# Performance work log

Measured on AMD Instinct MI355X. Metric: run time of the kernel, lower is better.

Reference implementation:

```python
import jax, jax.numpy as jnp
import numpy as np

EPS = 1e-5

def layernorm(x, g, b):
    mu = jnp.mean(x, axis=-1, keepdims=True)
    var = jnp.mean(jnp.square(x - mu), axis=-1, keepdims=True)
    return (x - mu) * jax.lax.rsqrt(var + EPS) * g + b

def setup_inputs() -> dict:
    key = jax.random.key(0)
    ks = jax.random.split(key, 12)
    B, V, P, C = 2, 8192, 16, 256
    FFN_IN, FFN_HID = 2 * C, 2 * C * 4
    s = 0.02
    return {
        "source": jax.random.normal(ks[0], (B, V, C), jnp.float32),
        "target": jax.random.normal(ks[1], (B, V, P, C), jnp.float32),
        "weights": jax.random.uniform(ks[2], (B, V, P), jnp.float32),
        "confidences": jax.random.uniform(ks[3], (B, V, P), jnp.float32),
        "Wq": jax.random.normal(ks[4], (C, C), jnp.float32) * s,
        "Wk": jax.random.normal(ks[5], (C, C), jnp.float32) * s,
        "Wv": jax.random.normal(ks[6], (C, C), jnp.float32) * s,
        "Wm": jax.random.normal(ks[7], (C, C), jnp.float32) * s,
        "g1": jnp.ones((C,), jnp.float32),
        "b1": jnp.zeros((C,), jnp.float32),
        "Wf1": jax.random.normal(ks[8], (FFN_IN, FFN_HID), jnp.float32) * s,
        "Wf2": jax.random.normal(ks[9], (FFN_HID, C), jnp.float32) * s,
        "g2": jnp.ones((C,), jnp.float32),
        "b2": jnp.zeros((C,), jnp.float32),
    }

NUM_HEAD = 8

def reference(source, target, weights, confidences, Wq, Wk, Wv, Wm, g1, b1, Wf1, Wf2, g2, b2):
    B, V, P, C = target.shape
    H = NUM_HEAD
    D = C // H
    # projections (bias-free linears)
    q = (source @ Wq).reshape(B, V, H, D)          # [B,V,H,D]
    k = (target @ Wk).reshape(B, V, P, H, D)       # [B,V,P,H,D]
    v = (target @ Wv).reshape(B, V, P, H, D)
    # scores scaled by per-neighbor weights then softmax over P
    scores = jnp.einsum("bvhd,bvphd->bvhp", q, k) * weights[:, :, None, :] / jnp.sqrt(jnp.float32(D))
    attn = jax.nn.softmax(scores, axis=-1)          # [B,V,H,P]
    # confidence-scaled weighted sum over neighbors
    out = jnp.einsum("bvhp,bvp,bvphd->bvhd", attn, confidences, v).reshape(B, V, C)
    message = layernorm(out @ Wm, g1, b1)
    h = jnp.concatenate([source, message], axis=-1) @ Wf1
    message = layernorm(jax.nn.gelu(h, approximate=False) @ Wf2, g2, b2)
    return source + message
```

## Files before the change

### kernel.cpp

```cpp
#include <hip/hip_runtime.h>
#include <hip/hip_bf16.h>
#include <math.h>

#define T_TOK 16384
#define CC 256
#define PP 16
#define HH 8
#define DD 32
#define LN_EPS 1e-5f

typedef __attribute__((ext_vector_type(8))) short bf16x8_t;
typedef __attribute__((ext_vector_type(4))) float f32x4_t;

__device__ __forceinline__ unsigned short f2bf(float x) {
  __hip_bfloat16 h = __float2bfloat16(x);
  return *reinterpret_cast<unsigned short*>(&h);
}
__device__ __forceinline__ float bf2f(unsigned short u) {
  union { unsigned int i; float f; } v; v.i = ((unsigned int)u) << 16; return v.f;
}
__device__ __forceinline__ void gl_lds16(const unsigned short* g, unsigned short* l) {
  __builtin_amdgcn_global_load_lds(
      (const __attribute__((address_space(1))) unsigned int*)g,
      (__attribute__((address_space(3))) unsigned int*)l, 16, 0, 0);
}

__global__ __launch_bounds__(256) void cvt_bf16_kernel(const float* __restrict__ src,
                                                       unsigned short* __restrict__ dst) {
  int i = (blockIdx.x * 256 + threadIdx.x) * 4;
  float4 v = *(const float4*)&src[i];
  ushort4 o = make_ushort4(f2bf(v.x), f2bf(v.y), f2bf(v.z), f2bf(v.w));
  *(ushort4*)&dst[i] = o;
}

__global__ __launch_bounds__(256) void transpose_cvt_kernel(const float* __restrict__ src,
                                                            unsigned short* __restrict__ dst,
                                                            int K, int N) {
  __shared__ float tile[64][65];
  int k0 = blockIdx.x * 64, n0 = blockIdx.y * 64;
  int tid = threadIdx.x;
#pragma unroll
  for (int i = 0; i < 16; i++) {
    int lin = i * 256 + tid, r = lin >> 6, c = lin & 63;
    tile[r][c] = src[(size_t)(k0 + r) * N + n0 + c];
  }
  __syncthreads();
#pragma unroll
  for (int i = 0; i < 16; i++) {
    int lin = i * 256 + tid, n = lin >> 6, k = lin & 63;
    dst[(size_t)(n0 + n) * K + k0 + k] = f2bf(tile[k][n]);
  }
}

__global__ __launch_bounds__(256) void precM_kernel(const float* __restrict__ Wq,
                                                    const float* __restrict__ Wk,
                                                    unsigned short* __restrict__ Mt) {
  __shared__ float wqS[256][33];
  __shared__ float wkS[128][33];
  const int tid = threadIdx.x;
  const int h = blockIdx.x >> 1, eh = blockIdx.x & 1;
#pragma unroll
  for (int it = 0; it < 32; it++) {
    int lin = it * 256 + tid, r = lin >> 5, d = lin & 31;
    wqS[r][d] = Wq[(size_t)r * CC + h * DD + d];
  }
#pragma unroll
  for (int it = 0; it < 16; it++) {
    int lin = it * 256 + tid, r = lin >> 5, d = lin & 31;
    wkS[r][d] = Wk[(size_t)(eh * 128 + r) * CC + h * DD + d];
  }
  __syncthreads();
  const int w = tid >> 6, l = tid & 63;
  for (int ei = 0; ei < 32; ei++) {
    int e = w * 32 + ei;
    float o[4] = {0.f, 0.f, 0.f, 0.f};
#pragma unroll
    for (int d = 0; d < 32; d++) {
      float kv = wkS[e][d];
      o[0] += kv * wqS[l][d];
      o[1] += kv * wqS[l + 64][d];
      o[2] += kv * wqS[l + 128][d];
      o[3] += kv * wqS[l + 192][d];
    }
    size_t rowb = (size_t)(h * 256 + eh * 128 + e) * CC;
    Mt[rowb + l] = f2bf(o[0]);
    Mt[rowb + l + 64] = f2bf(o[1]);
    Mt[rowb + l + 128] = f2bf(o[2]);
    Mt[rowb + l + 192] = f2bf(o[3]);
  }
}

__global__ __launch_bounds__(256) void precWVM_kernel(const float* __restrict__ Wv,
                                                      const float* __restrict__ Wm,
                                                      unsigned short* __restrict__ WVMt) {
  __shared__ float WvS[256][33];
  __shared__ float WmS[32][257];
  const int h = blockIdx.x;
  const int tid = threadIdx.x;
#pragma unroll
  for (int it = 0; it < 32; it++) {
    int lin = it * 256 + tid, e = lin >> 5, d = lin & 31;
    WvS[e][d] = Wv[(size_t)e * CC + h * DD + d];
  }
#pragma unroll
  for (int it = 0; it < 32; it++) {
    int lin = it * 256 + tid, d = lin >> 8, c = lin & 255;
    WmS[d][c] = Wm[(size_t)(h * DD + d) * CC + c];
  }
  __syncthreads();
  float wm[32];
#pragma unroll
  for (int d = 0; d < 32; d++) wm[d] = WmS[d][tid];
  for (int e = 0; e < 256; e++) {
    float acc = 0.f;
#pragma unroll
    for (int d = 0; d < 32; d++) acc += WvS[e][d] * wm[d];
    WVMt[(size_t)tid * 2048 + h * 256 + e] = f2bf(acc);
  }
}

__global__ __launch_bounds__(512) void qk_gemm_kernel(
    const unsigned short* __restrict__ A, const unsigned short* __restrict__ Bt,
    unsigned short* __restrict__ Out, int K, int strideO) {
  __shared__ __align__(16) unsigned short As[64 * 64];
  __shared__ __align__(16) unsigned short Bs[256 * 64];
  const int tid = threadIdx.x;
  const int wv = tid >> 6, l = tid & 63;
  const int wr = wv >> 2, wc = wv & 3;
  const int lr = l & 15, lq = l >> 4;
  const int m0 = blockIdx.x * 64;
  const int n0 = blockIdx.y * 256;
  const int nsteps = K >> 6;

  f32x4_t acc[2][4];
#pragma unroll
  for (int m = 0; m < 2; m++)
#pragma unroll
    for (int n = 0; n < 4; n++) acc[m][n] = (f32x4_t){0.f, 0.f, 0.f, 0.f};

  const int rS = tid >> 3, sS = tid & 7, qS = sS ^ (rS & 7);

  for (int st = 0; st < nsteps; st++) {
    int kn = st * 64;
    gl_lds16(&A[(size_t)(m0 + rS) * K + kn + qS * 8], &As[tid * 8]);
#pragma unroll
    for (int it = 0; it < 4; it++) {
      int lin = it * 512 + tid, r = lin >> 3, s = lin & 7, q = s ^ (r & 7);
      gl_lds16(&Bt[(size_t)(n0 + r) * K + kn + q * 8], &Bs[lin * 8]);
    }
    __syncthreads();
#pragma unroll
    for (int kk = 0; kk < 2; kk++) {
      bf16x8_t af[2], bfr[4];
#pragma unroll
      for (int m = 0; m < 2; m++) {
        int r = wr * 32 + m * 16 + lr;
        int slot = (kk * 4 + lq) ^ (r & 7);
        af[m] = *(const bf16x8_t*)&As[r * 64 + slot * 8];
      }
#pragma unroll
      for (int n = 0; n < 4; n++) {
        int r = wc * 64 + n * 16 + lr;
        int slot = (kk * 4 + lq) ^ (r & 7);
        bfr[n] = *(const bf16x8_t*)&Bs[r * 64 + slot * 8];
      }
#pragma unroll
      for (int m = 0; m < 2; m++)
#pragma unroll
        for (int n = 0; n < 4; n++)
          acc[m][n] = __builtin_amdgcn_mfma_f32_16x16x32_bf16(af[m], bfr[n], acc[m][n], 0, 0, 0);
    }
    __syncthreads();
  }

#pragma unroll
  for (int m = 0; m < 2; m++)
#pragma unroll
    for (int n = 0; n < 4; n++)
#pragma unroll
      for (int j = 0; j < 4; j++) {
        int rl = wr * 32 + m * 16 + lq * 4 + j;
        int col = n0 + wc * 64 + n * 16 + lr;
        Out[(size_t)(m0 + rl) * strideO + col] = f2bf(acc[m][n][j]);
      }
}

__global__ __launch_bounds__(256) void gemm128_kernel(
    const unsigned short* __restrict__ A, const unsigned short* __restrict__ A2,
    const unsigned short* __restrict__ Bt, unsigned short* __restrict__ Out,
    int K, int strideO) {
  __shared__ __align__(16) unsigned short As[128 * 64];
  __shared__ __align__(16) unsigned short Bs[128 * 64];
  const int tid = threadIdx.x;
  const int wv = tid >> 6, l = tid & 63;
  const int wr = wv >> 1, wc = wv & 1;
  const int lr = l & 15, lq = l >> 4;
  const int m0 = blockIdx.x * 128;
  const int n0 = blockIdx.y * 128;
  const int nsteps = K >> 6;

  f32x4_t acc[4][4];
#pragma unroll
  for (int m = 0; m < 4; m++)
#pragma unroll
    for (int n = 0; n < 4; n++) acc[m][n] = (f32x4_t){0.f, 0.f, 0.f, 0.f};

  for (int st = 0; st < nsteps; st++) {
    int kn = st * 64;
#pragma unroll
    for (int it = 0; it < 4; it++) {
      int lin = it * 256 + tid, r = lin >> 3, s = lin & 7, q = s ^ (r & 7);
      int ka = kn + q * 8;
      const unsigned short* ap = (ka < 256) ? &A[(size_t)(m0 + r) * CC + ka]
                                            : &A2[(size_t)(m0 + r) * CC + ka - 256];
      gl_lds16(ap, &As[lin * 8]);
      gl_lds16(&Bt[(size_t)(n0 + r) * K + kn + q * 8], &Bs[lin * 8]);
    }
    __syncthreads();
#pragma unroll
    for (int kk = 0; kk < 2; kk++) {
      bf16x8_t af[4], bf[4];
#pragma unroll
      for (int m = 0; m < 4; m++) {
        int r = wr * 64 + m * 16 + lr;
        int slot = (kk * 4 + lq) ^ (r & 7);
        af[m] = *(const bf16x8_t*)&As[r * 64 + slot * 8];
      }
#pragma unroll
      for (int n = 0; n < 4; n++) {
        int r = wc * 64 + n * 16 + lr;
        int slot = (kk * 4 + lq) ^ (r & 7);
        bf[n] = *(const bf16x8_t*)&Bs[r * 64 + slot * 8];
      }
#pragma unroll
      for (int m = 0; m < 4; m++)
#pragma unroll
        for (int n = 0; n < 4; n++)
          acc[m][n] = __builtin_amdgcn_mfma_f32_16x16x32_bf16(af[m], bf[n], acc[m][n], 0, 0, 0);
    }
    __syncthreads();
  }

#pragma unroll
  for (int m = 0; m < 4; m++)
#pragma unroll
    for (int n = 0; n < 4; n++)
#pragma unroll
      for (int j = 0; j < 4; j++) {
        int row = m0 + wr * 64 + m * 16 + lq * 4 + j;
        int col = n0 + wc * 64 + n * 16 + lr;
        float x = acc[m][n][j];
        x = 0.5f * x * (1.0f + erff(x * 0.70710678118654752f));
        Out[(size_t)row * strideO + col] = f2bf(x);
      }
}

__global__ __launch_bounds__(256) void attn2_kernel(const unsigned short* __restrict__ QKc,
                                                    const float* __restrict__ target,
                                                    const float* __restrict__ wts,
                                                    const float* __restrict__ conf,
                                                    unsigned short* __restrict__ TC) {
  __shared__ __align__(16) unsigned short Ts[4][16 * 256];
  __shared__ float awL[4][PP][HH];
  const int tid = threadIdx.x;
  const int w = tid >> 6, l = tid & 63;
  const int t = blockIdx.x * 4 + w;
  const float* trow = target + (size_t)t * PP * CC;
  char* tsb = (char*)&Ts[w][0];

  {
    const int p = l >> 2;
#pragma unroll
    for (int i = 0; i < 8; i++) {
      int s = (l & 3) + i * 4;
      const float* gp = &trow[p * CC + s * 8];
      float4 v0 = *(const float4*)gp;
      float4 v1 = *(const float4*)(gp + 4);
      ushort4 u0 = make_ushort4(f2bf(v0.x), f2bf(v0.y), f2bf(v0.z), f2bf(v0.w));
      ushort4 u1 = make_ushort4(f2bf(v1.x), f2bf(v1.y), f2bf(v1.z), f2bf(v1.w));
      uint4 pk;
      pk.x = (unsigned)u0.x | ((unsigned)u0.y << 16);
      pk.y = (unsigned)u0.z | ((unsigned)u0.w << 16);
      pk.z = (unsigned)u1.x | ((unsigned)u1.y << 16);
      pk.w = (unsigned)u1.z | ((unsigned)u1.w << 16);
      *(uint4*)(tsb + p * 512 + ((s ^ (p & 7)) << 4)) = pk;
    }
  }

  f32x4_t sc4 = (f32x4_t){0.f, 0.f, 0.f, 0.f};
  {
    const int lr = l & 15, lq = l >> 4;
    const unsigned short* qkrow = QKc + (size_t)t * 2048 + (size_t)(lr & 7) * 256;
#pragma unroll
    for (int es = 0; es < 8; es++) {
      int slot = es * 4 + lq;
      bf16x8_t aF = *(const bf16x8_t*)(tsb + lr * 512 + ((slot ^ (lr & 7)) << 4));
      bf16x8_t bF = *(const bf16x8_t*)&qkrow[es * 32 + lq * 8];
      sc4 = __builtin_amdgcn_mfma_f32_16x16x32_bf16(aF, bF, sc4, 0, 0, 0);
    }
  }

  {
    const int g = l >> 4;
    const float rsD = 0.17677669529663687f;
    float sc[4], cf[4];
#pragma unroll
    for (int j = 0; j < 4; j++) {
      int p = g * 4 + j;
      sc[j] = sc4[j] * wts[(size_t)t * PP + p] * rsD;
      cf[j] = conf[(size_t)t * PP + p];
    }
    float mx = fmaxf(fmaxf(sc[0], sc[1]), fmaxf(sc[2], sc[3]));
    mx = fmaxf(mx, __shfl_xor(mx, 16, 64));
    mx = fmaxf(mx, __shfl_xor(mx, 32, 64));
    float ex[4], sm = 0.f;
#pragma unroll
    for (int j = 0; j < 4; j++) { ex[j] = expf(sc[j] - mx); sm += ex[j]; }
    sm += __shfl_xor(sm, 16, 64);
    sm += __shfl_xor(sm, 32, 64);
    float inv = 1.f / sm;
    if ((l & 15) < 8) {
#pragma unroll
      for (int j = 0; j < 4; j++) awL[w][g * 4 + j][l & 15] = ex[j] * inv * cf[j];
    }
  }

  float tc[HH][4];
#pragma unroll
  for (int h = 0; h < HH; h++)
#pragma unroll
    for (int j = 0; j < 4; j++) tc[h][j] = 0.f;
#pragma unroll
  for (int p = 0; p < PP; p++) {
    uint2 tv = *(const uint2*)(tsb + p * 512 + (((l >> 1) ^ (p & 7)) << 4) + (l & 1) * 8);
    float te0 = bf2f((unsigned short)(tv.x & 0xffff));
    float te1 = bf2f((unsigned short)(tv.x >> 16));
    float te2 = bf2f((unsigned short)(tv.y & 0xffff));
    float te3 = bf2f((unsigned short)(tv.y >> 16));
#pragma unroll
    for (int h = 0; h < HH; h++) {
      float a = awL[w][p][h];
      tc[h][0] += a * te0; tc[h][1] += a * te1;
      tc[h][2] += a * te2; tc[h][3] += a * te3;
    }
  }
  size_t tcb = (size_t)t * 2048;
#pragma unroll
  for (int h = 0; h < HH; h++) {
    ushort4 o = make_ushort4(f2bf(tc[h][0]), f2bf(tc[h][1]), f2bf(tc[h][2]), f2bf(tc[h][3]));
    *(ushort4*)&TC[tcb + h * 256 + 4 * l] = o;
  }
}

template<int EPI>
__global__ __launch_bounds__(256) void nwide_gemm_kernel(
    const unsigned short* __restrict__ A, const unsigned short* __restrict__ Bt,
    unsigned short* __restrict__ OutB, float* __restrict__ OutF,
    const float* __restrict__ gam, const float* __restrict__ bet,
    const float* __restrict__ res) {
  __shared__ __align__(16) unsigned short As[32 * 64];
  __shared__ __align__(16) unsigned short Bs[256 * 64];
  __shared__ float redS[32][5], redQ[32][5];
  const int tid = threadIdx.x;
  const int wc = tid >> 6, l = tid & 63;
  const int lr = l & 15, lq = l >> 4;
  const int m0 = blockIdx.x * 32;
  const int K = 2048;

  f32x4_t acc[2][4];
#pragma unroll
  for (int m = 0; m < 2; m++)
#pragma unroll
    for (int n = 0; n < 4; n++) acc[m][n] = (f32x4_t){0.f, 0.f, 0.f, 0.f};

  const int rS = tid >> 3, sS = tid & 7, qS = sS ^ (rS & 7);

  for (int st = 0; st < 32; st++) {
    int kn = st * 64;
    gl_lds16(&A[(size_t)(m0 + rS) * K + kn + qS * 8], &As[tid * 8]);
#pragma unroll
    for (int it = 0; it < 8; it++) {
      int lin = it * 256 + tid, r = lin >> 3, s = lin & 7, q = s ^ (r & 7);
      gl_lds16(&Bt[(size_t)r * K + kn + q * 8], &Bs[lin * 8]);
    }
    __syncthreads();
#pragma unroll
    for (int kk = 0; kk < 2; kk++) {
      bf16x8_t af[2], bfr[4];
#pragma unroll
      for (int m = 0; m < 2; m++) {
        int r = m * 16 + lr;
        int slot = (kk * 4 + lq) ^ (r & 7);
        af[m] = *(const bf16x8_t*)&As[r * 64 + slot * 8];
      }
#pragma unroll
      for (int n = 0; n < 4; n++) {
        int r = wc * 64 + n * 16 + lr;
        int slot = (kk * 4 + lq) ^ (r & 7);
        bfr[n] = *(const bf16x8_t*)&Bs[r * 64 + slot * 8];
      }
#pragma unroll
      for (int m = 0; m < 2; m++)
#pragma unroll
        for (int n = 0; n < 4; n++)
          acc[m][n] = __builtin_amdgcn_mfma_f32_16x16x32_bf16(af[m], bfr[n], acc[m][n], 0, 0, 0);
    }
    __syncthreads();
  }

  float s1[2][4], s2[2][4];
#pragma unroll
  for (int m = 0; m < 2; m++)
#pragma unroll
    for (int j = 0; j < 4; j++) {
      float a = 0.f, b = 0.f;
#pragma unroll
      for (int n = 0; n < 4; n++) { float x = acc[m][n][j]; a += x; b += x * x; }
      s1[m][j] = a; s2[m][j] = b;
    }
#pragma unroll
  for (int mask = 1; mask < 16; mask <<= 1)
#pragma unroll
    for (int m = 0; m < 2; m++)
#pragma unroll
      for (int j = 0; j < 4; j++) {
        s1[m][j] += __shfl_xor(s1[m][j], mask, 64);
        s2[m][j] += __shfl_xor(s2[m][j], mask, 64);
      }
  if (lr == 0) {
#pragma unroll
    for (int m = 0; m < 2; m++)
#pragma unroll
      for (int j = 0; j < 4; j++) {
        int rl = m * 16 + lq * 4 + j;
        redS[rl][wc] = s1[m][j];
        redQ[rl][wc] = s2[m][j];
      }
  }
  __syncthreads();
#pragma unroll
  for (int m = 0; m < 2; m++)
#pragma unroll
    for (int j = 0; j < 4; j++) {
      int rl = m * 16 + lq * 4 + j;
      float ts = redS[rl][0] + redS[rl][1] + redS[rl][2] + redS[rl][3];
      float tq = redQ[rl][0] + redQ[rl][1] + redQ[rl][2] + redQ[rl][3];
      float mu = ts * (1.f / 256.f);
      float var = tq * (1.f / 256.f) - mu * mu;
      float rs = rsqrtf(var + LN_EPS);
      size_t rowg = (size_t)(m0 + rl);
#pragma unroll
      for (int n = 0; n < 4; n++) {
        int col = wc * 64 + n * 16 + lr;
        float v = (acc[m][n][j] - mu) * rs * gam[col] + bet[col];
        if constexpr (EPI == 0) {
          OutB[rowg * CC + col] = f2bf(v);
        } else {
          OutF[rowg * CC + col] = res[rowg * CC + col] + v;
        }
      }
    }
}

extern "C" void kernel_launch(void* const* d_in, const int* in_sizes, int n_in,
                              void* d_out, int out_size, void* d_ws, size_t ws_size,
                              hipStream_t stream) {
  const float* source = (const float*)d_in[0];
  const float* target = (const float*)d_in[1];
  const float* weights = (const float*)d_in[2];
  const float* conf   = (const float*)d_in[3];
  const float* Wq = (const float*)d_in[4];
  const float* Wk = (const float*)d_in[5];
  const float* Wv = (const float*)d_in[6];
  const float* Wm = (const float*)d_in[7];
  const float* g1 = (const float*)d_in[8];
  const float* b1 = (const float*)d_in[9];
  const float* Wf1 = (const float*)d_in[10];
  const float* Wf2 = (const float*)d_in[11];
  const float* g2 = (const float*)d_in[12];
  const float* b2 = (const float*)d_in[13];
  float* out = (float*)d_out;

  unsigned short* SB   = (unsigned short*)d_ws;
  unsigned short* MSGb = SB + (size_t)T_TOK * CC;
  unsigned short* Mt   = MSGb + (size_t)T_TOK * CC;
  unsigned short* WVMt = Mt + (size_t)2048 * 256;
  unsigned short* WF1t = WVMt + (size_t)256 * 2048;
  unsigned short* WF2t = WF1t + (size_t)2048 * 512;
  unsigned short* BIG1 = WF2t + (size_t)256 * 2048;
  unsigned short* BIG2 = BIG1 + (size_t)T_TOK * 2048;
  unsigned short* QKc  = BIG1;
  unsigned short* hid  = BIG1;
  unsigned short* TC   = BIG2;

  cvt_bf16_kernel<<<T_TOK * CC / 1024, 256, 0, stream>>>(source, SB);
  transpose_cvt_kernel<<<dim3(8, 32), 256, 0, stream>>>(Wf1, WF1t, 512, 2048);
  transpose_cvt_kernel<<<dim3(32, 4), 256, 0, stream>>>(Wf2, WF2t, 2048, 256);
  precM_kernel<<<16, 256, 0, stream>>>(Wq, Wk, Mt);
  precWVM_kernel<<<8, 256, 0, stream>>>(Wv, Wm, WVMt);

  qk_gemm_kernel<<<dim3(T_TOK / 64, 8), 512, 0, stream>>>(SB, Mt, QKc, 256, 2048);
  attn2_kernel<<<T_TOK / 4, 256, 0, stream>>>(QKc, target, weights, conf, TC);
  nwide_gemm_kernel<0><<<T_TOK / 32, 256, 0, stream>>>(
      TC, WVMt, MSGb, nullptr, g1, b1, nullptr);

  gemm128_kernel<<<dim3(T_TOK / 128, 16), 256, 0, stream>>>(
      SB, MSGb, WF1t, hid, 512, 2048);
  nwide_gemm_kernel<1><<<T_TOK / 32, 256, 0, stream>>>(
      hid, WF2t, nullptr, out, g2, b2, source);
}
```

Before: 328.2 us.

## Merge weight-prep kernels into one launch and double nwide GEMM K-step

Four small weight-preparation kernels (two transposes and two weight-product precomputes) are folded into a single launch that dispatches on block index, removing three launch gaps. Separately, the nwide GEMM now stages 128-wide K slices per iteration instead of 64, with an XOR swizzle over 16 slots, halving the number of barrier-separated steps. The larger LDS footprint (about 72KB per block) reduces how many blocks fit per CU, and the fused prep kernel's 66KB static shared buffer also limits its occupancy.

```diff
diff --git a/kernel.cpp b/kernel.cpp
--- a/kernel.cpp
+++ b/kernel.cpp
@@ -33,89 +33,90 @@
   *(ushort4*)&dst[i] = o;
 }
 
-__global__ __launch_bounds__(256) void transpose_cvt_kernel(const float* __restrict__ src,
-                                                            unsigned short* __restrict__ dst,
-                                                            int K, int N) {
-  __shared__ float tile[64][65];
-  int k0 = blockIdx.x * 64, n0 = blockIdx.y * 64;
-  int tid = threadIdx.x;
-#pragma unroll
-  for (int i = 0; i < 16; i++) {
-    int lin = i * 256 + tid, r = lin >> 6, c = lin & 63;
-    tile[r][c] = src[(size_t)(k0 + r) * N + n0 + c];
-  }
-  __syncthreads();
-#pragma unroll
-  for (int i = 0; i < 16; i++) {
-    int lin = i * 256 + tid, n = lin >> 6, k = lin & 63;
-    dst[(size_t)(n0 + n) * K + k0 + k] = f2bf(tile[k][n]);
-  }
-}
-
-__global__ __launch_bounds__(256) void precM_kernel(const float* __restrict__ Wq,
-                                                    const float* __restrict__ Wk,
-                                                    unsigned short* __restrict__ Mt) {
-  __shared__ float wqS[256][33];
-  __shared__ float wkS[128][33];
+__global__ __launch_bounds__(256) void prep_small_kernel(
+    const float* __restrict__ Wf1, const float* __restrict__ Wf2,
+    const float* __restrict__ Wq, const float* __restrict__ Wk,
+    const float* __restrict__ Wv, const float* __restrict__ Wm,
+    unsigned short* __restrict__ WF1t, unsigned short* __restrict__ WF2t,
+    unsigned short* __restrict__ Mt, unsigned short* __restrict__ WVMt) {
+  __shared__ __align__(16) char smem[66688];
+  const int b = blockIdx.x;
   const int tid = threadIdx.x;
-  const int h = blockIdx.x >> 1, eh = blockIdx.x & 1;
-#pragma unroll
-  for (int it = 0; it < 32; it++) {
-    int lin = it * 256 + tid, r = lin >> 5, d = lin & 31;
-    wqS[r][d] = Wq[(size_t)r * CC + h * DD + d];
-  }
-#pragma unroll
-  for (int it = 0; it < 16; it++) {
-    int lin = it * 256 + tid, r = lin >> 5, d = lin & 31;
-    wkS[r][d] = Wk[(size_t)(eh * 128 + r) * CC + h * DD + d];
-  }
-  __syncthreads();
-  const int w = tid >> 6, l = tid & 63;
-  for (int ei = 0; ei < 32; ei++) {
-    int e = w * 32 + ei;
-    float o[4] = {0.f, 0.f, 0.f, 0.f};
-#pragma unroll
-    for (int d = 0; d < 32; d++) {
-      float kv = wkS[e][d];
-      o[0] += kv * wqS[l][d];
-      o[1] += kv * wqS[l + 64][d];
-      o[2] += kv * wqS[l + 128][d];
-      o[3] += kv * wqS[l + 192][d];
-    }
-    size_t rowb = (size_t)(h * 256 + eh * 128 + e) * CC;
-    Mt[rowb + l] = f2bf(o[0]);
-    Mt[rowb + l + 64] = f2bf(o[1]);
-    Mt[rowb + l + 128] = f2bf(o[2]);
-    Mt[rowb + l + 192] = f2bf(o[3]);
-  }
-}
-
-__global__ __launch_bounds__(256) void precWVM_kernel(const float* __restrict__ Wv,
-                                                      const float* __restrict__ Wm,
-                                                      unsigned short* __restrict__ WVMt) {
-  __shared__ float WvS[256][33];
-  __shared__ float WmS[32][257];
-  const int h = blockIdx.x;
-  const int tid = threadIdx.x;
-#pragma unroll
-  for (int it = 0; it < 32; it++) {
-    int lin = it * 256 + tid, e = lin >> 5, d = lin & 31;
-    WvS[e][d] = Wv[(size_t)e * CC + h * DD + d];
-  }
-#pragma unroll
-  for (int it = 0; it < 32; it++) {
-    int lin = it * 256 + tid, d = lin >> 8, c = lin & 255;
-    WmS[d][c] = Wm[(size_t)(h * DD + d) * CC + c];
-  }
-  __syncthreads();
-  float wm[32];
-#pragma unroll
-  for (int d = 0; d < 32; d++) wm[d] = WmS[d][tid];
-  for (int e = 0; e < 256; e++) {
-    float acc = 0.f;
-#pragma unroll
-    for (int d = 0; d < 32; d++) acc += WvS[e][d] * wm[d];
-    WVMt[(size_t)tid * 2048 + h * 256 + e] = f2bf(acc);
+
+  if (b < 384) {
+    const float* src; unsigned short* dst; int K, N, k0, n0;
+    if (b < 256) { src = Wf1; dst = WF1t; K = 512;  N = 2048; k0 = (b & 7) * 64;  n0 = (b >> 3) * 64; }
+    else { int bb = b - 256; src = Wf2; dst = WF2t; K = 2048; N = 256;  k0 = (bb & 31) * 64; n0 = (bb >> 5) * 64; }
+    float (*tile)[65] = (float (*)[65])smem;
+#pragma unroll
+    for (int i = 0; i < 16; i++) {
+      int lin = i * 256 + tid, r = lin >> 6, c = lin & 63;
+      tile[r][c] = src[(size_t)(k0 + r) * N + n0 + c];
+    }
+    __syncthreads();
+#pragma unroll
+    for (int i = 0; i < 16; i++) {
+      int lin = i * 256 + tid, n = lin >> 6, k = lin & 63;
+      dst[(size_t)(n0 + n) * K + k0 + k] = f2bf(tile[k][n]);
+    }
+  } else if (b < 400) {
+    const int hb = b - 384;
+    const int h = hb >> 1, eh = hb & 1;
+    float (*wqS)[33] = (float (*)[33])smem;
+    float (*wkS)[33] = (float (*)[33])(smem + 256 * 33 * 4);
+#pragma unroll
+    for (int it = 0; it < 32; it++) {
+      int lin = it * 256 + tid, r = lin >> 5, d = lin & 31;
+      wqS[r][d] = Wq[(size_t)r * CC + h * DD + d];
+    }
+#pragma unroll
+    for (int it = 0; it < 16; it++) {
+      int lin = it * 256 + tid, r = lin >> 5, d = lin & 31;
+      wkS[r][d] = Wk[(size_t)(eh * 128 + r) * CC + h * DD + d];
+    }
+    __syncthreads();
+    const int w = tid >> 6, l = tid & 63;
+    for (int ei = 0; ei < 32; ei++) {
+      int e = w * 32 + ei;
+      float o[4] = {0.f, 0.f, 0.f, 0.f};
+#pragma unroll
+      for (int d = 0; d < 32; d++) {
+        float kv = wkS[e][d];
+        o[0] += kv * wqS[l][d];
+        o[1] += kv * wqS[l + 64][d];
+        o[2] += kv * wqS[l + 128][d];
+        o[3] += kv * wqS[l + 192][d];
+      }
+      size_t rowb = (size_t)(h * 256 + eh * 128 + e) * CC;
+      Mt[rowb + l] = f2bf(o[0]);
+      Mt[rowb + l + 64] = f2bf(o[1]);
+      Mt[rowb + l + 128] = f2bf(o[2]);
+      Mt[rowb + l + 192] = f2bf(o[3]);
+    }
+  } else {
+    const int h = b - 400;
+    float (*WvS)[33] = (float (*)[33])smem;
+    float (*WmS)[257] = (float (*)[257])(smem + 256 * 33 * 4);
+#pragma unroll
+    for (int it = 0; it < 32; it++) {
+      int lin = it * 256 + tid, e = lin >> 5, d = lin & 31;
+      WvS[e][d] = Wv[(size_t)e * CC + h * DD + d];
+    }
+#pragma unroll
+    for (int it = 0; it < 32; it++) {
+      int lin = it * 256 + tid, d = lin >> 8, c = lin & 255;
+      WmS[d][c] = Wm[(size_t)(h * DD + d) * CC + c];
+    }
+    __syncthreads();
+    float wm[32];
+#pragma unroll
+    for (int d = 0; d < 32; d++) wm[d] = WmS[d][tid];
+    for (int e = 0; e < 256; e++) {
+      float acc = 0.f;
+#pragma unroll
+      for (int d = 0; d < 32; d++) acc += WvS[e][d] * wm[d];
+      WVMt[(size_t)tid * 2048 + h * 256 + e] = f2bf(acc);
+    }
   }
 }
 
@@ -358,8 +359,8 @@
     unsigned short* __restrict__ OutB, float* __restrict__ OutF,
     const float* __restrict__ gam, const float* __restrict__ bet,
     const float* __restrict__ res) {
-  __shared__ __align__(16) unsigned short As[32 * 64];
-  __shared__ __align__(16) unsigned short Bs[256 * 64];
+  __shared__ __align__(16) unsigned short As[32 * 128];
+  __shared__ __align__(16) unsigned short Bs[256 * 128];
   __shared__ float redS[32][5], redQ[32][5];
   const int tid = threadIdx.x;
   const int wc = tid >> 6, l = tid & 63;
@@ -373,31 +374,33 @@
 #pragma unroll
     for (int n = 0; n < 4; n++) acc[m][n] = (f32x4_t){0.f, 0.f, 0.f, 0.f};
 
-  const int rS = tid >> 3, sS = tid & 7, qS = sS ^ (rS & 7);
-
-  for (int st = 0; st < 32; st++) {
-    int kn = st * 64;
-    gl_lds16(&A[(size_t)(m0 + rS) * K + kn + qS * 8], &As[tid * 8]);
-#pragma unroll
-    for (int it = 0; it < 8; it++) {
-      int lin = it * 256 + tid, r = lin >> 3, s = lin & 7, q = s ^ (r & 7);
+  for (int st = 0; st < 16; st++) {
+    int kn = st * 128;
+#pragma unroll
+    for (int it = 0; it < 2; it++) {
+      int lin = it * 256 + tid, r = lin >> 4, s = lin & 15, q = s ^ (r & 15);
+      gl_lds16(&A[(size_t)(m0 + r) * K + kn + q * 8], &As[lin * 8]);
+    }
+#pragma unroll
+    for (int it = 0; it < 16; it++) {
+      int lin = it * 256 + tid, r = lin >> 4, s = lin & 15, q = s ^ (r & 15);
       gl_lds16(&Bt[(size_t)r * K + kn + q * 8], &Bs[lin * 8]);
     }
     __syncthreads();
 #pragma unroll
-    for (int kk = 0; kk < 2; kk++) {
+    for (int kk = 0; kk < 4; kk++) {
       bf16x8_t af[2], bfr[4];
 #pragma unroll
       for (int m = 0; m < 2; m++) {
         int r = m * 16 + lr;
-        int slot = (kk * 4 + lq) ^ (r & 7);
-        af[m] = *(const bf16x8_t*)&As[r * 64 + slot * 8];
+        int slot = (kk * 4 + lq) ^ (r & 15);
+        af[m] = *(const bf16x8_t*)&As[r * 128 + slot * 8];
       }
 #pragma unroll
       for (int n = 0; n < 4; n++) {
         int r = wc * 64 + n * 16 + lr;
-        int slot = (kk * 4 + lq) ^ (r & 7);
-        bfr[n] = *(const bf16x8_t*)&Bs[r * 64 + slot * 8];
+        int slot = (kk * 4 + lq) ^ (r & 15);
+        bfr[n] = *(const bf16x8_t*)&Bs[r * 128 + slot * 8];
       }
 #pragma unroll
       for (int m = 0; m < 2; m++)
@@ -494,10 +497,8 @@
   unsigned short* TC   = BIG2;
 
   cvt_bf16_kernel<<<T_TOK * CC / 1024, 256, 0, stream>>>(source, SB);
-  transpose_cvt_kernel<<<dim3(8, 32), 256, 0, stream>>>(Wf1, WF1t, 512, 2048);
-  transpose_cvt_kernel<<<dim3(32, 4), 256, 0, stream>>>(Wf2, WF2t, 2048, 256);
-  precM_kernel<<<16, 256, 0, stream>>>(Wq, Wk, Mt);
-  precWVM_kernel<<<8, 256, 0, stream>>>(Wv, Wm, WVMt);
+  prep_small_kernel<<<408, 256, 0, stream>>>(Wf1, Wf2, Wq, Wk, Wv, Wm,
+                                             WF1t, WF2t, Mt, WVMt);
 
   qk_gemm_kernel<<<dim3(T_TOK / 64, 8), 512, 0, stream>>>(SB, Mt, QKc, 256, 2048);
   attn2_kernel<<<T_TOK / 4, 256, 0, stream>>>(QKc, target, weights, conf, TC);
```

After: 302.7 us. 7.8% less time.
